# Performance work log

Measured on AMD Instinct MI355X. Metric: run time of the kernel, lower is better.

## Reference

```python
import jax, jax.numpy as jnp
import numpy as np


def log_g(x):
    # Appendix B.3 of 'Were RNNs All We Needed?'
    return jnp.where(x >= 0, jnp.log(jax.nn.relu(x) + 0.5), -jax.nn.softplus(-x))


def parallel_scan_log(log_a, log_b):
    # h[0] = b[0]; h[i] = a[i]*h[i-1] + b[i], computed in log space along axis 1
    log_a_star = jnp.cumsum(log_a, axis=1)
    log_x0_plus_b_star = jax.lax.cumlogsumexp(log_b - log_a_star, axis=1)
    return jnp.exp(log_a_star + log_x0_plus_b_star)


def setup_inputs() -> dict:
    key = jax.random.key(0)
    B, T, D = 8, 4096, 1024
    k1, k2, k3, k4, k5 = jax.random.split(key, 5)
    scale = 1.0 / np.sqrt(D)
    return {
        "h_prev_layer": jax.random.normal(k1, (B, T, D), dtype=jnp.float32),
        "W_z": jax.random.uniform(k2, (D, D), jnp.float32, -scale, scale),
        "b_z": jax.random.uniform(k3, (D,), jnp.float32, -scale, scale),
        "W_h": jax.random.uniform(k4, (D, D), jnp.float32, -scale, scale),
        "b_h": jax.random.uniform(k5, (D,), jnp.float32, -scale, scale),
    }


def reference(h_prev_layer, W_z, b_z, W_h, b_h):
    k = jnp.einsum('btd,ed->bte', h_prev_layer, W_z) + b_z          # linear_z
    tilde_h = jnp.einsum('btd,ed->bte', h_prev_layer, W_h) + b_h    # linear_h
    log_z = -jax.nn.softplus(-k)
    log_one_minus_z = -jax.nn.softplus(k)
    log_tilde_h = log_g(tilde_h)
    return parallel_scan_log(log_one_minus_z, log_z + log_tilde_h)
```

## Files before the change

### kernel.cpp

```cpp
#include <hip/hip_runtime.h>
#include <hip/hip_fp16.h>

typedef float f32x4 __attribute__((ext_vector_type(4)));
typedef __bf16 bf16x8 __attribute__((ext_vector_type(8)));

#define BB_ 8
#define TT_ 4096
#define DD_ 1024
#define MM_ (BB_*TT_)
#define KK_ DD_

#define NCH 64
#define LCH (TT_/NCH)

static __device__ __forceinline__ unsigned short f2bf_rn(float f) {
  unsigned int u = __float_as_uint(f);
  u += 0x7FFFu + ((u >> 16) & 1u);
  return (unsigned short)(u >> 16);
}

__global__ void cvt_f32_bf16(const float4* __restrict__ src,
                             ushort4* __restrict__ dst, int n4) {
  int stride = gridDim.x * blockDim.x;
  for (int i = blockIdx.x * blockDim.x + threadIdx.x; i < n4; i += stride) {
    float4 v = src[i];
    ushort4 o;
    o.x = f2bf_rn(v.x); o.y = f2bf_rn(v.y);
    o.z = f2bf_rn(v.z); o.w = f2bf_rn(v.w);
    dst[i] = o;
  }
}

__device__ __forceinline__ void gload_lds16(const void* g, void* l) {
  __builtin_amdgcn_global_load_lds(
      (const __attribute__((address_space(1))) void*)g,
      (__attribute__((address_space(3))) void*)l, 16, 0, 0);
}

#define STA(q, nb_, kkh) gload_lds16(pXa + (q) * 65536 + (kkh), (nb_) + (q) * 8192 + wofs)
#define STB(q, nb_, kkh) gload_lds16(pWb + (q) * 65536 + (kkh), (nb_) + 32768 + (q) * 8192 + wofs)

#define LOADF(DA, DB, base_, mh, kh) do {                                   \
    const char* A__ = (base_);                                              \
    const char* B__ = (base_) + 32768;                                      \
    const int s__ = (kh) ? sk1 : sk0;                                       \
    _Pragma("unroll")                                                       \
    for (int ii = 0; ii < 4; ++ii)                                          \
      DA[ii] = *reinterpret_cast<const bf16x8*>(                            \
          A__ + rA7 + (mh) * 8192 + ii * 2048 + s__);                       \
    _Pragma("unroll")                                                       \
    for (int j = 0; j < 4; ++j)                                             \
      DB[j] = *reinterpret_cast<const bf16x8*>(B__ + rB7 + j * 2048 + s__); \
  } while (0)

#define MFMAQ(SA, SB, mh) do {                                              \
    __builtin_amdgcn_s_setprio(1);                                          \
    _Pragma("unroll")                                                       \
    for (int ii = 0; ii < 4; ++ii)                                          \
      _Pragma("unroll")                                                     \
      for (int j = 0; j < 4; ++j)                                           \
        acc[(mh) * 4 + ii][j] = __builtin_amdgcn_mfma_f32_16x16x32_bf16(    \
            SA[ii], SB[j], acc[(mh) * 4 + ii][j], 0, 0, 0);                 \
    __builtin_amdgcn_s_setprio(0);                                          \
  } while (0)

#define BARSB() do { __builtin_amdgcn_s_barrier();                          \
                     __builtin_amdgcn_sched_barrier(0); } while (0)
#define LGKM8() do { asm volatile("s_waitcnt lgkmcnt(8)" ::: "memory");     \
                     __builtin_amdgcn_sched_barrier(0); } while (0)
#define LGKM0() do { asm volatile("s_waitcnt lgkmcnt(0)" ::: "memory");     \
                     __builtin_amdgcn_sched_barrier(0); } while (0)
#define VM0()   asm volatile("s_waitcnt vmcnt(0)" ::: "memory")

__global__ __launch_bounds__(512, 2) void gemm_fused(
    const unsigned short* __restrict__ Xb,
    const unsigned short* __restrict__ Wb,
    const float* __restrict__ bz, const float* __restrict__ bh,
    __half* __restrict__ Zb, __half* __restrict__ Gb)
{
  extern __shared__ __align__(16) char smem[];
  const int tid  = threadIdx.x;
  const int wave = tid >> 6;
  const int lane = tid & 63;
  const int wm = wave >> 2, wn = wave & 3;
  const int fr = lane & 15, kg = lane >> 4, fx = fr & 7;

  int swz = (blockIdx.x & 7) * 128 + (blockIdx.x >> 3);
  const int m0 = (swz >> 3) * 256;
  const int e0 = (swz & 7) * 256;

  const int arow = tid >> 3;
  const int aslx = ((tid & 7) ^ (arow & 7)) * 8;
  const unsigned short* pXa = Xb + (size_t)(m0 + arow) * KK_ + aslx;
  const unsigned short* pWb = Wb + (size_t)(e0 + arow) * KK_ + aslx;
  const int wofs = wave * 1024;

  const int rA7 = (wm * 128 + fr) * 128;
  const int rB7 = (wn * 64 + fr) * 128;
  const int sk0 = (kg ^ fx) * 16;
  const int sk1 = sk0 ^ 64;

  f32x4 acc[8][4];
  #pragma unroll
  for (int i = 0; i < 8; i++)
    #pragma unroll
    for (int j = 0; j < 4; j++)
      acc[i][j] = (f32x4){0.f, 0.f, 0.f, 0.f};
  bf16x8 afA[4], bvA[4], afB[4], bvB[4];

  STA(0, smem, 0); STA(1, smem, 0); STA(2, smem, 0); STA(3, smem, 0);
  STB(0, smem, 0); STB(1, smem, 0); STB(2, smem, 0); STB(3, smem, 0);
  VM0();
  __builtin_amdgcn_s_barrier();
  LOADF(afA, bvA, smem, 0, 0);

  #pragma unroll 1
  for (int t = 0; t < 15; ++t) {
    char* cb = smem + ((t & 1) << 16);
    char* nb = smem + (((t + 1) & 1) << 16);
    const int kn = (t + 1) * 64;
    BARSB();
    LOADF(afB, bvB, cb, 1, 0);
    STA(0, nb, kn); STA(1, nb, kn); STA(2, nb, kn); STA(3, nb, kn);
    STB(0, nb, kn); STB(1, nb, kn); STB(2, nb, kn); STB(3, nb, kn);
    LGKM8();
    MFMAQ(afA, bvA, 0);
    BARSB();
    LOADF(afA, bvA, cb, 0, 1);
    LGKM8();
    MFMAQ(afB, bvB, 1);
    BARSB();
    LOADF(afB, bvB, cb, 1, 1);
    VM0();
    LGKM8();
    MFMAQ(afA, bvA, 0);
    BARSB();
    LOADF(afA, bvA, nb, 0, 0);
    LGKM8();
    MFMAQ(afB, bvB, 1);
  }
  {
    char* cb = smem + 65536;
    BARSB(); LOADF(afB, bvB, cb, 1, 0); LGKM8(); MFMAQ(afA, bvA, 0);
    BARSB(); LOADF(afA, bvA, cb, 0, 1); LGKM8(); MFMAQ(afB, bvB, 1);
    BARSB(); LOADF(afB, bvB, cb, 1, 1); LGKM8(); MFMAQ(afA, bvA, 0);
    BARSB(); LGKM0();                   MFMAQ(afB, bvB, 1);
    __builtin_amdgcn_s_barrier();
  }

  const bool isZ = (e0 < DD_);
  const float* bias = isZ ? bz : bh;
  __half* outp = isZ ? Zb : Gb;
  const int ec0 = (isZ ? e0 : (e0 - DD_)) + wn * 64;

  float bv[4];
  #pragma unroll
  for (int j = 0; j < 4; j++) bv[j] = bias[ec0 + j * 16 + fr];

  __half* ew = (__half*)(smem + wave * 9216);
  const int sub = lane & 7, rowr = lane >> 3;

  #pragma unroll
  for (int p = 0; p < 2; ++p) {
    #pragma unroll
    for (int ii = 0; ii < 4; ++ii) {
      #pragma unroll
      for (int j = 0; j < 4; ++j) {
        #pragma unroll
        for (int r = 0; r < 4; ++r) {
          float val = acc[p * 4 + ii][j][r] + bv[j];
          float res;
          if (isZ) {
            res = 1.0f / (1.0f + __expf(-val));
          } else {
            res = (val >= 0.0f) ? (val + 0.5f)
                                : (1.0f / (1.0f + __expf(-val)));
          }
          ew[(ii * 16 + kg * 4 + r) * 72 + j * 16 + fr] = __float2half(res);
        }
      }
    }
    #pragma unroll
    for (int q = 0; q < 8; ++q) {
      int rl = q * 8 + rowr;
      uint4 v = *reinterpret_cast<const uint4*>(&ew[rl * 72 + sub * 8]);
      size_t rg = (size_t)(m0 + wm * 128 + p * 64 + rl);
      *reinterpret_cast<uint4*>(&outp[rg * DD_ + ec0 + sub * 8]) = v;
    }
  }
}

__global__ __launch_bounds__(256) void scan_partial(
    const ushort4* __restrict__ Z, const ushort4* __restrict__ G,
    float4* __restrict__ P, float4* __restrict__ Q) {
  const int d4 = threadIdx.x;
  const int c  = blockIdx.x;
  const int b  = blockIdx.y;
  size_t base = ((size_t)b * TT_ + (size_t)c * LCH) * (DD_ / 4) + d4;
  float p0=1.f,p1=1.f,p2=1.f,p3=1.f, q0=0.f,q1=0.f,q2=0.f,q3=0.f;
  for (int t = 0; t < LCH; ++t) {
    ushort4 uz = Z[base + (size_t)t * (DD_ / 4)];
    ushort4 ug = G[base + (size_t)t * (DD_ / 4)];
    float z, g, a;
    z = __half2float(__ushort_as_half(uz.x)); g = __half2float(__ushort_as_half(ug.x));
    a = 1.f - z; p0 *= a; q0 = fmaf(a, q0, z * g);
    z = __half2float(__ushort_as_half(uz.y)); g = __half2float(__ushort_as_half(ug.y));
    a = 1.f - z; p1 *= a; q1 = fmaf(a, q1, z * g);
    z = __half2float(__ushort_as_half(uz.z)); g = __half2float(__ushort_as_half(ug.z));
    a = 1.f - z; p2 *= a; q2 = fmaf(a, q2, z * g);
    z = __half2float(__ushort_as_half(uz.w)); g = __half2float(__ushort_as_half(ug.w));
    a = 1.f - z; p3 *= a; q3 = fmaf(a, q3, z * g);
  }
  size_t o = ((size_t)b * NCH + c) * (DD_ / 4) + d4;
  P[o] = make_float4(p0, p1, p2, p3);
  Q[o] = make_float4(q0, q1, q2, q3);
}

__global__ __launch_bounds__(256) void scan_combine(
    const float4* __restrict__ P, const float4* __restrict__ Q,
    float4* __restrict__ H) {
  const int d4 = threadIdx.x;
  const int b  = blockIdx.x;
  float4 h = make_float4(0.f, 0.f, 0.f, 0.f);
  for (int c = 0; c < NCH; ++c) {
    size_t o = ((size_t)b * NCH + c) * (DD_ / 4) + d4;
    H[o] = h;
    float4 p = P[o], q = Q[o];
    h.x = fmaf(p.x, h.x, q.x);
    h.y = fmaf(p.y, h.y, q.y);
    h.z = fmaf(p.z, h.z, q.z);
    h.w = fmaf(p.w, h.w, q.w);
  }
}

__global__ __launch_bounds__(256) void scan_apply(
    const ushort4* __restrict__ Z, const ushort4* __restrict__ G,
    const float4* __restrict__ H, float4* __restrict__ out) {
  const int d4 = threadIdx.x;
  const int c  = blockIdx.x;
  const int b  = blockIdx.y;
  float4 h = H[((size_t)b * NCH + c) * (DD_ / 4) + d4];
  size_t base = ((size_t)b * TT_ + (size_t)c * LCH) * (DD_ / 4) + d4;
  for (int t = 0; t < LCH; ++t) {
    ushort4 uz = Z[base + (size_t)t * (DD_ / 4)];
    ushort4 ug = G[base + (size_t)t * (DD_ / 4)];
    float z, g, a;
    z = __half2float(__ushort_as_half(uz.x)); g = __half2float(__ushort_as_half(ug.x));
    a = 1.f - z; h.x = fmaf(a, h.x, z * g);
    z = __half2float(__ushort_as_half(uz.y)); g = __half2float(__ushort_as_half(ug.y));
    a = 1.f - z; h.y = fmaf(a, h.y, z * g);
    z = __half2float(__ushort_as_half(uz.z)); g = __half2float(__ushort_as_half(ug.z));
    a = 1.f - z; h.z = fmaf(a, h.z, z * g);
    z = __half2float(__ushort_as_half(uz.w)); g = __half2float(__ushort_as_half(ug.w));
    a = 1.f - z; h.w = fmaf(a, h.w, z * g);
    out[base + (size_t)t * (DD_ / 4)] = h;
  }
}

extern "C" void kernel_launch(void* const* d_in, const int* in_sizes, int n_in,
                              void* d_out, int out_size, void* d_ws, size_t ws_size,
                              hipStream_t stream) {
  const float* X  = (const float*)d_in[0];
  const float* Wz = (const float*)d_in[1];
  const float* bz = (const float*)d_in[2];
  const float* Wh = (const float*)d_in[3];
  const float* bh = (const float*)d_in[4];
  float* out = (float*)d_out;

  const size_t szXb = (size_t)MM_ * DD_ * 2;
  const size_t szWb = (size_t)2 * DD_ * DD_ * 2;
  const size_t szZ  = (size_t)MM_ * DD_ * 2;
  const size_t szPQ = (size_t)BB_ * NCH * DD_ * 4;

  char* ws = (char*)d_ws;
  unsigned short *Xb, *Wb;
  __half *Zb, *Gb;
  const size_t needA = szXb + szWb + 2 * szZ + 3 * szPQ;
  if (ws_size >= needA) {
    Xb = (unsigned short*)ws;              ws += szXb;
    Wb = (unsigned short*)ws;              ws += szWb;
  } else {
    Xb = (unsigned short*)d_out;
    Wb = (unsigned short*)((char*)d_out + szXb);
  }
  Zb = (__half*)ws;  ws += szZ;
  Gb = (__half*)ws;  ws += szZ;
  float* P = (float*)ws;  ws += szPQ;
  float* Q = (float*)ws;  ws += szPQ;
  float* H = (float*)ws;

  cvt_f32_bf16<<<2048, 256, 0, stream>>>((const float4*)X, (ushort4*)Xb,
                                         (int)((size_t)MM_ * DD_ / 4));
  cvt_f32_bf16<<<512, 256, 0, stream>>>((const float4*)Wz, (ushort4*)Wb,
                                        DD_ * DD_ / 4);
  cvt_f32_bf16<<<512, 256, 0, stream>>>((const float4*)Wh,
                                        (ushort4*)(Wb + (size_t)DD_ * DD_),
                                        DD_ * DD_ / 4);
  gemm_fused<<<(MM_ / 256) * ((2 * DD_) / 256), 512, 131072, stream>>>(
      Xb, Wb, bz, bh, Zb, Gb);

  scan_partial<<<dim3(NCH, BB_), 256, 0, stream>>>((const ushort4*)Zb, (const ushort4*)Gb,
                                                   (float4*)P, (float4*)Q);
  scan_combine<<<BB_, 256, 0, stream>>>((const float4*)P, (const float4*)Q, (float4*)H);
  scan_apply<<<dim3(NCH, BB_), 256, 0, stream>>>((const ushort4*)Zb, (const ushort4*)Gb,
                                                 (const float4*)H, (float4*)out);
}
```

Before: 300.2 us.

## Switch GEMM to 32x32x16 MFMA with asm LDS reads; widen scan_combine grid

The GEMM inner loop moves from 16x16x32 MFMA tiles to 32x32x16 bf16 MFMA, with new LDS read addressing, inline-asm ds_read_b128, a reworked register double-buffer schedule and adjusted lgkmcnt waits. The larger tile is meant to cut LDS read traffic and instruction count per FLOP. The epilogue remaps accumulator rows for the 32x32 layout and adds barriers around the staging buffer. Separately, scan_combine goes from 8 blocks of float4 work to 32 blocks of scalar work to expose more parallelism in that serial stage.

```diff
diff --git a/kernel.cpp b/kernel.cpp
--- a/kernel.cpp
+++ b/kernel.cpp
@@ -2,7 +2,10 @@
 #include <hip/hip_fp16.h>
 
 typedef float f32x4 __attribute__((ext_vector_type(4)));
+typedef float f32x16 __attribute__((ext_vector_type(16)));
 typedef __bf16 bf16x8 __attribute__((ext_vector_type(8)));
+typedef unsigned int u32x4 __attribute__((ext_vector_type(4)));
+typedef __attribute__((address_space(3))) const void* lds_cp;
 
 #define BB_ 8
 #define TT_ 4096
@@ -40,36 +43,44 @@
 #define STA(q, nb_, kkh) gload_lds16(pXa + (q) * 65536 + (kkh), (nb_) + (q) * 8192 + wofs)
 #define STB(q, nb_, kkh) gload_lds16(pWb + (q) * 65536 + (kkh), (nb_) + 32768 + (q) * 8192 + wofs)
 
-#define LOADF(DA, DB, base_, mh, kh) do {                                   \
-    const char* A__ = (base_);                                              \
-    const char* B__ = (base_) + 32768;                                      \
-    const int s__ = (kh) ? sk1 : sk0;                                       \
-    _Pragma("unroll")                                                       \
-    for (int ii = 0; ii < 4; ++ii)                                          \
-      DA[ii] = *reinterpret_cast<const bf16x8*>(                            \
-          A__ + rA7 + (mh) * 8192 + ii * 2048 + s__);                       \
-    _Pragma("unroll")                                                       \
-    for (int j = 0; j < 4; ++j)                                             \
-      DB[j] = *reinterpret_cast<const bf16x8*>(B__ + rB7 + j * 2048 + s__); \
+#define DSR(dst, gp) \
+  asm volatile("ds_read_b128 %0, %1" : "=&v"(dst) : "v"((lds_cp)(gp)))
+
+#define RD_A(SET, mh, kh, bp) do {                                \
+    DSR(SET[0], (bp) + rbA[(mh)*2+0] + ck[(kh)*2+0]);             \
+    DSR(SET[1], (bp) + rbA[(mh)*2+0] + ck[(kh)*2+1]);             \
+    DSR(SET[2], (bp) + rbA[(mh)*2+1] + ck[(kh)*2+0]);             \
+    DSR(SET[3], (bp) + rbA[(mh)*2+1] + ck[(kh)*2+1]);             \
   } while (0)
-
-#define MFMAQ(SA, SB, mh) do {                                              \
-    __builtin_amdgcn_s_setprio(1);                                          \
-    _Pragma("unroll")                                                       \
-    for (int ii = 0; ii < 4; ++ii)                                          \
-      _Pragma("unroll")                                                     \
-      for (int j = 0; j < 4; ++j)                                           \
-        acc[(mh) * 4 + ii][j] = __builtin_amdgcn_mfma_f32_16x16x32_bf16(    \
-            SA[ii], SB[j], acc[(mh) * 4 + ii][j], 0, 0, 0);                 \
-    __builtin_amdgcn_s_setprio(0);                                          \
+#define RD_B(SET, kh, bp) do {                                    \
+    DSR(SET[0], (bp) + rbB[0] + ck[(kh)*2+0]);                    \
+    DSR(SET[1], (bp) + rbB[0] + ck[(kh)*2+1]);                    \
+    DSR(SET[2], (bp) + rbB[1] + ck[(kh)*2+0]);                    \
+    DSR(SET[3], (bp) + rbB[1] + ck[(kh)*2+1]);                    \
   } while (0)
 
-#define BARSB() do { __builtin_amdgcn_s_barrier();                          \
+#define BC(x) __builtin_bit_cast(bf16x8, x)
+#define MFMA8(ASET, BSET, mh) do {                                              \
+    __builtin_amdgcn_s_setprio(1);                                              \
+    acc[(mh)*2+0][0] = __builtin_amdgcn_mfma_f32_32x32x16_bf16(BC(ASET[0]), BC(BSET[0]), acc[(mh)*2+0][0],0,0,0); \
+    acc[(mh)*2+0][0] = __builtin_amdgcn_mfma_f32_32x32x16_bf16(BC(ASET[1]), BC(BSET[1]), acc[(mh)*2+0][0],0,0,0); \
+    acc[(mh)*2+0][1] = __builtin_amdgcn_mfma_f32_32x32x16_bf16(BC(ASET[0]), BC(BSET[2]), acc[(mh)*2+0][1],0,0,0); \
+    acc[(mh)*2+0][1] = __builtin_amdgcn_mfma_f32_32x32x16_bf16(BC(ASET[1]), BC(BSET[3]), acc[(mh)*2+0][1],0,0,0); \
+    acc[(mh)*2+1][0] = __builtin_amdgcn_mfma_f32_32x32x16_bf16(BC(ASET[2]), BC(BSET[0]), acc[(mh)*2+1][0],0,0,0); \
+    acc[(mh)*2+1][0] = __builtin_amdgcn_mfma_f32_32x32x16_bf16(BC(ASET[3]), BC(BSET[1]), acc[(mh)*2+1][0],0,0,0); \
+    acc[(mh)*2+1][1] = __builtin_amdgcn_mfma_f32_32x32x16_bf16(BC(ASET[2]), BC(BSET[2]), acc[(mh)*2+1][1],0,0,0); \
+    acc[(mh)*2+1][1] = __builtin_amdgcn_mfma_f32_32x32x16_bf16(BC(ASET[3]), BC(BSET[3]), acc[(mh)*2+1][1],0,0,0); \
+    __builtin_amdgcn_s_setprio(0);                                              \
+  } while (0)
+
+#define BARSB() do { __builtin_amdgcn_s_barrier();                 \
                      __builtin_amdgcn_sched_barrier(0); } while (0)
-#define LGKM8() do { asm volatile("s_waitcnt lgkmcnt(8)" ::: "memory");     \
-                     __builtin_amdgcn_sched_barrier(0); } while (0)
-#define LGKM0() do { asm volatile("s_waitcnt lgkmcnt(0)" ::: "memory");     \
-                     __builtin_amdgcn_sched_barrier(0); } while (0)
+#define WAITLK8() do { asm volatile("s_waitcnt lgkmcnt(8)" ::: "memory"); \
+                       __builtin_amdgcn_sched_barrier(0); } while (0)
+#define WAITLK4() do { asm volatile("s_waitcnt lgkmcnt(4)" ::: "memory"); \
+                       __builtin_amdgcn_sched_barrier(0); } while (0)
+#define WAITLK0() do { asm volatile("s_waitcnt lgkmcnt(0)" ::: "memory"); \
+                       __builtin_amdgcn_sched_barrier(0); } while (0)
 #define VM0()   asm volatile("s_waitcnt vmcnt(0)" ::: "memory")
 
 __global__ __launch_bounds__(512, 2) void gemm_fused(
@@ -83,7 +94,7 @@
   const int wave = tid >> 6;
   const int lane = tid & 63;
   const int wm = wave >> 2, wn = wave & 3;
-  const int fr = lane & 15, kg = lane >> 4, fx = fr & 7;
+  const int ln31 = lane & 31, hi = lane >> 5, sw7 = ln31 & 7;
 
   int swz = (blockIdx.x & 7) * 128 + (blockIdx.x >> 3);
   const int m0 = (swz >> 3) * 256;
@@ -95,56 +106,67 @@
   const unsigned short* pWb = Wb + (size_t)(e0 + arow) * KK_ + aslx;
   const int wofs = wave * 1024;
 
-  const int rA7 = (wm * 128 + fr) * 128;
-  const int rB7 = (wn * 64 + fr) * 128;
-  const int sk0 = (kg ^ fx) * 16;
-  const int sk1 = sk0 ^ 64;
-
-  f32x4 acc[8][4];
-  #pragma unroll
-  for (int i = 0; i < 8; i++)
+  int rbA[4], rbB[2], ck[4];
+  #pragma unroll
+  for (int fm = 0; fm < 4; ++fm) rbA[fm] = (wm * 128 + fm * 32 + ln31) * 128;
+  #pragma unroll
+  for (int fn = 0; fn < 2; ++fn) rbB[fn] = 32768 + (wn * 64 + fn * 32 + ln31) * 128;
+  #pragma unroll
+  for (int ks = 0; ks < 4; ++ks) ck[ks] = ((ks * 2 + hi) ^ sw7) * 16;
+
+  f32x16 acc[4][2];
+  #pragma unroll
+  for (int i = 0; i < 4; i++)
     #pragma unroll
-    for (int j = 0; j < 4; j++)
-      acc[i][j] = (f32x4){0.f, 0.f, 0.f, 0.f};
-  bf16x8 afA[4], bvA[4], afB[4], bvB[4];
+    for (int j = 0; j < 2; j++)
+      acc[i][j] = (f32x16)(0.f);
+  u32x4 aP[4], aQ[4], bk0[4], bk1[4];
 
   STA(0, smem, 0); STA(1, smem, 0); STA(2, smem, 0); STA(3, smem, 0);
   STB(0, smem, 0); STB(1, smem, 0); STB(2, smem, 0); STB(3, smem, 0);
   VM0();
   __builtin_amdgcn_s_barrier();
-  LOADF(afA, bvA, smem, 0, 0);
+  RD_A(aP, 0, 0, smem);
+  RD_B(bk0, 0, smem);
 
   #pragma unroll 1
   for (int t = 0; t < 15; ++t) {
-    char* cb = smem + ((t & 1) << 16);
+    const char* cb = smem + ((t & 1) << 16);
     char* nb = smem + (((t + 1) & 1) << 16);
     const int kn = (t + 1) * 64;
     BARSB();
-    LOADF(afB, bvB, cb, 1, 0);
+    RD_A(aQ, 1, 0, cb); RD_B(bk1, 1, cb);
     STA(0, nb, kn); STA(1, nb, kn); STA(2, nb, kn); STA(3, nb, kn);
     STB(0, nb, kn); STB(1, nb, kn); STB(2, nb, kn); STB(3, nb, kn);
-    LGKM8();
-    MFMAQ(afA, bvA, 0);
-    BARSB();
-    LOADF(afA, bvA, cb, 0, 1);
-    LGKM8();
-    MFMAQ(afB, bvB, 1);
-    BARSB();
-    LOADF(afB, bvB, cb, 1, 1);
+    WAITLK8();
+    MFMA8(aP, bk0, 0);
+    BARSB();
+    RD_A(aP, 0, 1, cb);
+    WAITLK4();
+    MFMA8(aQ, bk0, 1);
+    BARSB();
+    RD_A(aQ, 1, 1, cb);
+    WAITLK4();
+    MFMA8(aP, bk1, 0);
     VM0();
-    LGKM8();
-    MFMAQ(afA, bvA, 0);
-    BARSB();
-    LOADF(afA, bvA, nb, 0, 0);
-    LGKM8();
-    MFMAQ(afB, bvB, 1);
+    BARSB();
+    RD_A(aP, 0, 0, nb); RD_B(bk0, 0, nb);
+    WAITLK8();
+    MFMA8(aQ, bk1, 1);
   }
   {
-    char* cb = smem + 65536;
-    BARSB(); LOADF(afB, bvB, cb, 1, 0); LGKM8(); MFMAQ(afA, bvA, 0);
-    BARSB(); LOADF(afA, bvA, cb, 0, 1); LGKM8(); MFMAQ(afB, bvB, 1);
-    BARSB(); LOADF(afB, bvB, cb, 1, 1); LGKM8(); MFMAQ(afA, bvA, 0);
-    BARSB(); LGKM0();                   MFMAQ(afB, bvB, 1);
+    const char* cb = smem + 65536;
+    BARSB();
+    RD_A(aQ, 1, 0, cb); RD_B(bk1, 1, cb);
+    WAITLK8(); MFMA8(aP, bk0, 0);
+    BARSB();
+    RD_A(aP, 0, 1, cb);
+    WAITLK4(); MFMA8(aQ, bk0, 1);
+    BARSB();
+    RD_A(aQ, 1, 1, cb);
+    WAITLK4(); MFMA8(aP, bk1, 0);
+    BARSB();
+    WAITLK0(); MFMA8(aQ, bk1, 1);
     __builtin_amdgcn_s_barrier();
   }
 
@@ -153,9 +175,9 @@
   __half* outp = isZ ? Zb : Gb;
   const int ec0 = (isZ ? e0 : (e0 - DD_)) + wn * 64;
 
-  float bv[4];
-  #pragma unroll
-  for (int j = 0; j < 4; j++) bv[j] = bias[ec0 + j * 16 + fr];
+  float bv[2];
+  #pragma unroll
+  for (int fn = 0; fn < 2; ++fn) bv[fn] = bias[ec0 + fn * 32 + ln31];
 
   __half* ew = (__half*)(smem + wave * 9216);
   const int sub = lane & 7, rowr = lane >> 3;
@@ -163,12 +185,12 @@
   #pragma unroll
   for (int p = 0; p < 2; ++p) {
     #pragma unroll
-    for (int ii = 0; ii < 4; ++ii) {
+    for (int f2 = 0; f2 < 2; ++f2) {
       #pragma unroll
-      for (int j = 0; j < 4; ++j) {
+      for (int fn = 0; fn < 2; ++fn) {
         #pragma unroll
-        for (int r = 0; r < 4; ++r) {
-          float val = acc[p * 4 + ii][j][r] + bv[j];
+        for (int r = 0; r < 16; ++r) {
+          float val = acc[p * 2 + f2][fn][r] + bv[fn];
           float res;
           if (isZ) {
             res = 1.0f / (1.0f + __expf(-val));
@@ -176,10 +198,12 @@
             res = (val >= 0.0f) ? (val + 0.5f)
                                 : (1.0f / (1.0f + __expf(-val)));
           }
-          ew[(ii * 16 + kg * 4 + r) * 72 + j * 16 + fr] = __float2half(res);
+          int rowf = (r & 3) + 8 * (r >> 2) + 4 * hi;
+          ew[(f2 * 32 + rowf) * 72 + fn * 32 + ln31] = __float2half(res);
         }
       }
     }
+    __builtin_amdgcn_s_barrier();
     #pragma unroll
     for (int q = 0; q < 8; ++q) {
       int rl = q * 8 + rowr;
@@ -187,6 +211,7 @@
       size_t rg = (size_t)(m0 + wm * 128 + p * 64 + rl);
       *reinterpret_cast<uint4*>(&outp[rg * DD_ + ec0 + sub * 8]) = v;
     }
+    __builtin_amdgcn_s_barrier();
   }
 }
 
@@ -217,19 +242,15 @@
 }
 
 __global__ __launch_bounds__(256) void scan_combine(
-    const float4* __restrict__ P, const float4* __restrict__ Q,
-    float4* __restrict__ H) {
-  const int d4 = threadIdx.x;
-  const int b  = blockIdx.x;
-  float4 h = make_float4(0.f, 0.f, 0.f, 0.f);
+    const float* __restrict__ P, const float* __restrict__ Q,
+    float* __restrict__ H) {
+  const int d = blockIdx.x * 256 + threadIdx.x;
+  const int b = blockIdx.y;
+  float h = 0.f;
   for (int c = 0; c < NCH; ++c) {
-    size_t o = ((size_t)b * NCH + c) * (DD_ / 4) + d4;
+    size_t o = ((size_t)b * NCH + c) * DD_ + d;
     H[o] = h;
-    float4 p = P[o], q = Q[o];
-    h.x = fmaf(p.x, h.x, q.x);
-    h.y = fmaf(p.y, h.y, q.y);
-    h.z = fmaf(p.z, h.z, q.z);
-    h.w = fmaf(p.w, h.w, q.w);
+    h = fmaf(P[o], h, Q[o]);
   }
 }
 
@@ -301,7 +322,7 @@
 
   scan_partial<<<dim3(NCH, BB_), 256, 0, stream>>>((const ushort4*)Zb, (const ushort4*)Gb,
                                                    (float4*)P, (float4*)Q);
-  scan_combine<<<BB_, 256, 0, stream>>>((const float4*)P, (const float4*)Q, (float4*)H);
+  scan_combine<<<dim3(4, BB_), 256, 0, stream>>>(P, Q, H);
   scan_apply<<<dim3(NCH, BB_), 256, 0, stream>>>((const ushort4*)Zb, (const ushort4*)Gb,
                                                  (const float4*)H, (float4*)out);
 }
```

After: 307.2 us. +2.3%, slower.
